# Optimization experiments

Hardware: AMD Instinct MI355X
Metric: run time of the kernel (lower is better)

Reference implementation:

```python
import jax, jax.numpy as jnp
import numpy as np

BN_EPS = 1e-5


def setup_inputs() -> dict:
    key = jax.random.key(0)
    k1, k2 = jax.random.split(key)
    B, IN, OUT = 16384, 2048, 2048
    x = jax.random.normal(k1, (B, IN), dtype=jnp.float32)
    weight = jax.random.normal(k2, (OUT, IN), dtype=jnp.float32) * 0.05
    gamma = jnp.ones((OUT,), dtype=jnp.float32)
    beta = jnp.zeros((OUT,), dtype=jnp.float32)
    return {"x": x, "weight": weight, "gamma": gamma, "beta": beta}


def reference(x, weight, gamma, beta):
    # Deterministic binarization: sign(w) in {-1, +1} (0 maps to +1)
    w_bin = jnp.where(weight >= 0, 1.0, -1.0).astype(weight.dtype)
    # Linear (no bias): y = x @ W_bin^T  -> [B, OUT]
    y = jnp.einsum("bi,oi->bo", x, w_bin)
    # BatchNorm1d, training mode: biased batch statistics over batch dim
    mean = jnp.mean(y, axis=0)
    var = jnp.mean(jnp.square(y - mean), axis=0)
    y = (y - mean) * (gamma * jax.lax.rsqrt(var + BN_EPS)) + beta
    # ReLU activation
    return jax.nn.relu(y)
```

## Files before the change

kernel.cpp:

```cpp
#include <hip/hip_runtime.h>
#include <stdint.h>

#define B_DIM   16384
#define IN_DIM  2048
#define OUT_DIM 2048
#define BN_EPS  1e-5f

typedef __bf16 bf16x8 __attribute__((ext_vector_type(8)));
typedef float  f32x4  __attribute__((ext_vector_type(4)));
typedef unsigned short u16x4 __attribute__((ext_vector_type(4)));
typedef unsigned short u16x8 __attribute__((ext_vector_type(8)));


__device__ __forceinline__ unsigned short f2bf_rne(float f) {
    unsigned u = __builtin_bit_cast(unsigned, f);
    return (unsigned short)((u + 0x7fffu + ((u >> 16) & 1u)) >> 16);
}
__device__ __forceinline__ float bf2f(unsigned short h) {
    unsigned u = ((unsigned)h) << 16;
    return __builtin_bit_cast(float, u);
}

__device__ __forceinline__ void gl_lds16(const __bf16* g, __bf16* l) {
    __builtin_amdgcn_global_load_lds(
        (const __attribute__((address_space(1))) unsigned int*)g,
        (__attribute__((address_space(3))) unsigned int*)l,
        16, 0, 0);
}

__global__ __launch_bounds__(256) void convert_x_kernel(
        const float4* __restrict__ x, u16x4* __restrict__ xb) {
    int id = blockIdx.x * 256 + threadIdx.x;
    float4 a = x[id];
    u16x4 o;
    o[0] = f2bf_rne(a.x); o[1] = f2bf_rne(a.y);
    o[2] = f2bf_rne(a.z); o[3] = f2bf_rne(a.w);
    xb[id] = o;
}

__global__ __launch_bounds__(256) void convert_w_kernel(
        const float4* __restrict__ w, u16x4* __restrict__ wb,
        float4* __restrict__ stats ) {
    int id = blockIdx.x * 256 + threadIdx.x;
    if (id < 1024) stats[id] = make_float4(0.f, 0.f, 0.f, 0.f);
    float4 a = w[id];
    u16x4 o;
    o[0] = (unsigned short)((a.x < 0.f) ? 0xBF80u : 0x3F80u);
    o[1] = (unsigned short)((a.y < 0.f) ? 0xBF80u : 0x3F80u);
    o[2] = (unsigned short)((a.z < 0.f) ? 0xBF80u : 0x3F80u);
    o[3] = (unsigned short)((a.w < 0.f) ? 0xBF80u : 0x3F80u);
    wb[id] = o;
}

template <bool BF16OUT>
__global__ __launch_bounds__(256, 2) void gemm_bn_kernel(
        const __bf16* __restrict__ A, const __bf16* __restrict__ Bw,
        unsigned short* __restrict__ Yb, float* __restrict__ Yf,
        float* __restrict__ colsum, float* __restrict__ colsumsq) {
    __shared__ __bf16 sA[128 * 32];
    __shared__ __bf16 sB[128 * 32];

    const int tid  = threadIdx.x;
    const int wave = tid >> 6;
    const int lane = tid & 63;
    const int wm = wave >> 1;
    const int wn = wave & 1;
    const int lr = lane & 15;
    const int lq = lane >> 4;

    const int b    = blockIdx.x;
    const int lb   = (b & 7) * 256 + (b >> 3);
    const int bm   = (lb >> 4) * 128;
    const int bn   = (lb & 15) * 128;

    const int srow = lane >> 2;
    const int scol = (lane & 3) * 8;
    const int chunk0 = wave * 2;
    const __bf16* ag0 = A  + (size_t)(bm + chunk0 * 16 + srow) * IN_DIM + scol;
    const __bf16* ag1 = ag0 + 16 * IN_DIM;
    const __bf16* bg0 = Bw + (size_t)(bn + chunk0 * 16 + srow) * IN_DIM + scol;
    const __bf16* bg1 = bg0 + 16 * IN_DIM;
    __bf16* la0 = sA + chunk0 * 512;
    __bf16* la1 = sA + (chunk0 + 1) * 512;
    __bf16* lb0 = sB + chunk0 * 512;
    __bf16* lb1 = sB + (chunk0 + 1) * 512;

    const int aoff = (wm * 64 + lr) * 32 + lq * 8;
    const int boff = (wn * 64 + lr) * 32 + lq * 8;

    f32x4 acc[4][4];
#pragma unroll
    for (int i = 0; i < 4; ++i)
#pragma unroll
        for (int j = 0; j < 4; ++j) {
            f32x4 z = {0.f, 0.f, 0.f, 0.f};
            acc[i][j] = z;
        }

    for (int k0 = 0; k0 < IN_DIM; k0 += 32) {
        __syncthreads();
        gl_lds16(ag0 + k0, la0);
        gl_lds16(ag1 + k0, la1);
        gl_lds16(bg0 + k0, lb0);
        gl_lds16(bg1 + k0, lb1);
        __syncthreads();

        bf16x8 av[4], bv[4];
#pragma unroll
        for (int i = 0; i < 4; ++i)
            av[i] = *(const bf16x8*)(sA + aoff + i * 512);
#pragma unroll
        for (int j = 0; j < 4; ++j)
            bv[j] = *(const bf16x8*)(sB + boff + j * 512);
#pragma unroll
        for (int i = 0; i < 4; ++i)
#pragma unroll
            for (int j = 0; j < 4; ++j)
                acc[i][j] = __builtin_amdgcn_mfma_f32_16x16x32_bf16(
                    av[i], bv[j], acc[i][j], 0, 0, 0);
    }

#pragma unroll
    for (int i = 0; i < 4; ++i) {
        int row0 = bm + wm * 64 + i * 16 + lq * 4;
#pragma unroll
        for (int r = 0; r < 4; ++r) {
            size_t base = (size_t)(row0 + r) * OUT_DIM + bn + wn * 64 + lr;
            if (BF16OUT) {
#pragma unroll
                for (int j = 0; j < 4; ++j)
                    Yb[base + j * 16] = f2bf_rne(acc[i][j][r]);
            } else {
#pragma unroll
                for (int j = 0; j < 4; ++j)
                    Yf[base + j * 16] = acc[i][j][r];
            }
        }
    }

#pragma unroll
    for (int j = 0; j < 4; ++j) {
        float s = 0.f, q = 0.f;
#pragma unroll
        for (int i = 0; i < 4; ++i)
#pragma unroll
            for (int r = 0; r < 4; ++r) {
                float v = acc[i][j][r];
                s += v;
                q += v * v;
            }
        s += __shfl_xor(s, 16); s += __shfl_xor(s, 32);
        q += __shfl_xor(q, 16); q += __shfl_xor(q, 32);
        if (lq == 0) {
            int col = bn + wn * 64 + j * 16 + lr;
            atomicAdd(&colsum[col], s);
            atomicAdd(&colsumsq[col], q);
        }
    }
}

__global__ __launch_bounds__(256) void finalize_kernel(
        const float* __restrict__ colsum, const float* __restrict__ colsumsq,
        const float* __restrict__ gamma, const float* __restrict__ beta,
        float* __restrict__ scale, float* __restrict__ bias) {
    int n = blockIdx.x * 256 + threadIdx.x;
    if (n < OUT_DIM) {
        const float inv = 1.f / (float)B_DIM;
        float mean = colsum[n] * inv;
        float var  = colsumsq[n] * inv - mean * mean;
        float sc   = gamma[n] * rsqrtf(var + BN_EPS);
        scale[n] = sc;
        bias[n]  = beta[n] - mean * sc;
    }
}

__global__ __launch_bounds__(256) void bn_relu_bf16_kernel(
        const u16x4* __restrict__ yb, float4* __restrict__ out,
        const float4* __restrict__ scale4, const float4* __restrict__ bias4) {
    int id = blockIdx.x * 256 + threadIdx.x;
    int c4 = id & (OUT_DIM / 4 - 1);
    u16x4 h = yb[id];
    float4 s = scale4[c4];
    float4 b = bias4[c4];
    float4 v;
    v.x = fmaxf(fmaf(bf2f(h[0]), s.x, b.x), 0.f);
    v.y = fmaxf(fmaf(bf2f(h[1]), s.y, b.y), 0.f);
    v.z = fmaxf(fmaf(bf2f(h[2]), s.z, b.z), 0.f);
    v.w = fmaxf(fmaf(bf2f(h[3]), s.w, b.w), 0.f);
    out[id] = v;
}

__global__ __launch_bounds__(256) void bn_relu_f32_kernel(
        float4* __restrict__ y, const float4* __restrict__ scale4,
        const float4* __restrict__ bias4) {
    int id = blockIdx.x * 256 + threadIdx.x;
    int c4 = id & (OUT_DIM / 4 - 1);
    float4 v = y[id];
    float4 s = scale4[c4];
    float4 b = bias4[c4];
    v.x = fmaxf(fmaf(v.x, s.x, b.x), 0.f);
    v.y = fmaxf(fmaf(v.y, s.y, b.y), 0.f);
    v.z = fmaxf(fmaf(v.z, s.z, b.z), 0.f);
    v.w = fmaxf(fmaf(v.w, s.w, b.w), 0.f);
    y[id] = v;
}

extern "C" void kernel_launch(void* const* d_in, const int* in_sizes, int n_in,
                              void* d_out, int out_size, void* d_ws, size_t ws_size,
                              hipStream_t stream) {
    const float* x     = (const float*)d_in[0];
    const float* w     = (const float*)d_in[1];
    const float* gamma = (const float*)d_in[2];
    const float* beta  = (const float*)d_in[3];
    float* out = (float*)d_out;

    char* ws = (char*)d_ws;
    const size_t XB_OFF = 0;
    const size_t WB_OFF = 67108864;
    const size_t YB_OFF = WB_OFF + 8388608;
    const size_t ST_OFF = YB_OFF + 67108864;
    const size_t NEED   = ST_OFF + 8192 * 4;

    __bf16* xb = (__bf16*)(ws + XB_OFF);
    __bf16* wb = (__bf16*)(ws + WB_OFF);
    unsigned short* yb = (unsigned short*)(ws + YB_OFF);
    bool use_bf16y = ws_size >= NEED;
    float* colsum = use_bf16y ? (float*)(ws + ST_OFF) : (float*)(ws + YB_OFF);
    float* colsumsq = colsum + 2048;
    float* scale    = colsum + 4096;
    float* bias     = colsum + 6144;

    convert_x_kernel<<<32768, 256, 0, stream>>>((const float4*)x, (u16x4*)xb);
    convert_w_kernel<<<4096, 256, 0, stream>>>((const float4*)w, (u16x4*)wb,
                                               (float4*)colsum);
    if (use_bf16y) {
        gemm_bn_kernel<true><<<2048, 256, 0, stream>>>(
            xb, wb, yb, out, colsum, colsumsq);
        finalize_kernel<<<8, 256, 0, stream>>>(colsum, colsumsq, gamma, beta,
                                               scale, bias);
        bn_relu_bf16_kernel<<<32768, 256, 0, stream>>>(
            (const u16x4*)yb, (float4*)out, (const float4*)scale,
            (const float4*)bias);
    } else {
        gemm_bn_kernel<false><<<2048, 256, 0, stream>>>(
            xb, wb, yb, out, colsum, colsumsq);
        finalize_kernel<<<8, 256, 0, stream>>>(colsum, colsumsq, gamma, beta,
                                               scale, bias);
        bn_relu_f32_kernel<<<32768, 256, 0, stream>>>(
            (float4*)out, (const float4*)scale, (const float4*)bias);
    }
}
```

Baseline: 406.9 us.

## Quantize activations to per-row int8 and use int8 MFMA for binary GEMM

Replaces the bf16 conversion of x with a per-row absmax int8 quantization kernel, and encodes the binarized weights as int8 ±1. The GEMM now uses the i32 16x16x64 int8 MFMA with a 64-wide K step, which halves the loop trip count and halves operand bytes. The row scale is applied in the epilogue before the bf16 store and the column statistics. The intent is to cut both matrix-core time and input conversion traffic. In exchange, activations are held at 8-bit precision, which adds quantization error to the outputs and the BN statistics, and the fp32 fallback path for small workspaces is removed.

```diff
diff --git a/kernel.cpp b/kernel.cpp
--- a/kernel.cpp
+++ b/kernel.cpp
@@ -6,10 +6,8 @@
 #define OUT_DIM 2048
 #define BN_EPS  1e-5f
 
-typedef __bf16 bf16x8 __attribute__((ext_vector_type(8)));
-typedef float  f32x4  __attribute__((ext_vector_type(4)));
+typedef int    i32x4 __attribute__((ext_vector_type(4)));
 typedef unsigned short u16x4 __attribute__((ext_vector_type(4)));
-typedef unsigned short u16x8 __attribute__((ext_vector_type(8)));
 
 
 __device__ __forceinline__ unsigned short f2bf_rne(float f) {
@@ -21,44 +19,65 @@
     return __builtin_bit_cast(float, u);
 }
 
-__device__ __forceinline__ void gl_lds16(const __bf16* g, __bf16* l) {
+__device__ __forceinline__ void gl_lds16(const void* g, void* l) {
     __builtin_amdgcn_global_load_lds(
         (const __attribute__((address_space(1))) unsigned int*)g,
         (__attribute__((address_space(3))) unsigned int*)l,
         16, 0, 0);
 }
 
-__global__ __launch_bounds__(256) void convert_x_kernel(
-        const float4* __restrict__ x, u16x4* __restrict__ xb) {
-    int id = blockIdx.x * 256 + threadIdx.x;
-    float4 a = x[id];
-    u16x4 o;
-    o[0] = f2bf_rne(a.x); o[1] = f2bf_rne(a.y);
-    o[2] = f2bf_rne(a.z); o[3] = f2bf_rne(a.w);
-    xb[id] = o;
+__device__ __forceinline__ int pack4(float a, float b, float c, float d, float inv) {
+    int q0 = (int)rintf(a * inv) & 255;
+    int q1 = (int)rintf(b * inv) & 255;
+    int q2 = (int)rintf(c * inv) & 255;
+    int q3 = (int)rintf(d * inv) & 255;
+    return q0 | (q1 << 8) | (q2 << 16) | (q3 << 24);
+}
+
+__global__ __launch_bounds__(256) void quantize_x_kernel(
+        const float4* __restrict__ x4, int* __restrict__ xq,
+        float* __restrict__ scales) {
+    __shared__ float wmax[4];
+    const int row = blockIdx.x;
+    const int t = threadIdx.x;
+    const float4* xr = x4 + (size_t)row * 512;
+    float4 a = xr[t];
+    float4 b = xr[t + 256];
+    float m = fmaxf(fmaxf(fabsf(a.x), fabsf(a.y)), fmaxf(fabsf(a.z), fabsf(a.w)));
+    m = fmaxf(m, fmaxf(fmaxf(fabsf(b.x), fabsf(b.y)), fmaxf(fabsf(b.z), fabsf(b.w))));
+#pragma unroll
+    for (int off = 32; off >= 1; off >>= 1) m = fmaxf(m, __shfl_xor(m, off));
+    if ((t & 63) == 0) wmax[t >> 6] = m;
+    __syncthreads();
+    m = fmaxf(fmaxf(wmax[0], wmax[1]), fmaxf(wmax[2], wmax[3]));
+    m = fmaxf(m, 1e-20f);
+    const float inv = 127.0f / m;
+    if (t == 0) scales[row] = m * (1.0f / 127.0f);
+    int* xo = xq + (size_t)row * 512;
+    xo[t]       = pack4(a.x, a.y, a.z, a.w, inv);
+    xo[t + 256] = pack4(b.x, b.y, b.z, b.w, inv);
 }
 
 __global__ __launch_bounds__(256) void convert_w_kernel(
-        const float4* __restrict__ w, u16x4* __restrict__ wb,
+        const float4* __restrict__ w, int* __restrict__ wq,
         float4* __restrict__ stats ) {
     int id = blockIdx.x * 256 + threadIdx.x;
     if (id < 1024) stats[id] = make_float4(0.f, 0.f, 0.f, 0.f);
     float4 a = w[id];
-    u16x4 o;
-    o[0] = (unsigned short)((a.x < 0.f) ? 0xBF80u : 0x3F80u);
-    o[1] = (unsigned short)((a.y < 0.f) ? 0xBF80u : 0x3F80u);
-    o[2] = (unsigned short)((a.z < 0.f) ? 0xBF80u : 0x3F80u);
-    o[3] = (unsigned short)((a.w < 0.f) ? 0xBF80u : 0x3F80u);
-    wb[id] = o;
-}
-
-template <bool BF16OUT>
+    int b0 = (a.x < 0.f) ? 0xFF : 0x01;
+    int b1 = (a.y < 0.f) ? 0xFF : 0x01;
+    int b2 = (a.z < 0.f) ? 0xFF : 0x01;
+    int b3 = (a.w < 0.f) ? 0xFF : 0x01;
+    wq[id] = b0 | (b1 << 8) | (b2 << 16) | (b3 << 24);
+}
+
 __global__ __launch_bounds__(256, 2) void gemm_bn_kernel(
-        const __bf16* __restrict__ A, const __bf16* __restrict__ Bw,
-        unsigned short* __restrict__ Yb, float* __restrict__ Yf,
+        const char* __restrict__ A, const char* __restrict__ Bw,
+        const float* __restrict__ scales,
+        unsigned short* __restrict__ Yb,
         float* __restrict__ colsum, float* __restrict__ colsumsq) {
-    __shared__ __bf16 sA[128 * 32];
-    __shared__ __bf16 sB[128 * 32];
+    __shared__ char sA[128 * 64];
+    __shared__ char sB[128 * 64];
 
     const int tid  = threadIdx.x;
     const int wave = tid >> 6;
@@ -68,36 +87,36 @@
     const int lr = lane & 15;
     const int lq = lane >> 4;
 
-    const int b    = blockIdx.x;
-    const int lb   = (b & 7) * 256 + (b >> 3);
-    const int bm   = (lb >> 4) * 128;
-    const int bn   = (lb & 15) * 128;
+    const int b  = blockIdx.x;
+    const int lb = (b & 7) * 256 + (b >> 3);
+    const int bm = (lb >> 4) * 128;
+    const int bn = (lb & 15) * 128;
 
     const int srow = lane >> 2;
-    const int scol = (lane & 3) * 8;
+    const int scol = (lane & 3) * 16;
     const int chunk0 = wave * 2;
-    const __bf16* ag0 = A  + (size_t)(bm + chunk0 * 16 + srow) * IN_DIM + scol;
-    const __bf16* ag1 = ag0 + 16 * IN_DIM;
-    const __bf16* bg0 = Bw + (size_t)(bn + chunk0 * 16 + srow) * IN_DIM + scol;
-    const __bf16* bg1 = bg0 + 16 * IN_DIM;
-    __bf16* la0 = sA + chunk0 * 512;
-    __bf16* la1 = sA + (chunk0 + 1) * 512;
-    __bf16* lb0 = sB + chunk0 * 512;
-    __bf16* lb1 = sB + (chunk0 + 1) * 512;
-
-    const int aoff = (wm * 64 + lr) * 32 + lq * 8;
-    const int boff = (wn * 64 + lr) * 32 + lq * 8;
-
-    f32x4 acc[4][4];
+    const char* ag0 = A  + (size_t)(bm + chunk0 * 16 + srow) * IN_DIM + scol;
+    const char* ag1 = ag0 + 16 * IN_DIM;
+    const char* bg0 = Bw + (size_t)(bn + chunk0 * 16 + srow) * IN_DIM + scol;
+    const char* bg1 = bg0 + 16 * IN_DIM;
+    char* la0 = sA + chunk0 * 1024;
+    char* la1 = sA + (chunk0 + 1) * 1024;
+    char* lb0 = sB + chunk0 * 1024;
+    char* lb1 = sB + (chunk0 + 1) * 1024;
+
+    const int aoff = (wm * 64 + lr) * 64 + lq * 16;
+    const int boff = (wn * 64 + lr) * 64 + lq * 16;
+
+    i32x4 acc[4][4];
 #pragma unroll
     for (int i = 0; i < 4; ++i)
 #pragma unroll
         for (int j = 0; j < 4; ++j) {
-            f32x4 z = {0.f, 0.f, 0.f, 0.f};
+            i32x4 z = {0, 0, 0, 0};
             acc[i][j] = z;
         }
 
-    for (int k0 = 0; k0 < IN_DIM; k0 += 32) {
+    for (int k0 = 0; k0 < IN_DIM; k0 += 64) {
         __syncthreads();
         gl_lds16(ag0 + k0, la0);
         gl_lds16(ag1 + k0, la1);
@@ -105,50 +124,47 @@
         gl_lds16(bg1 + k0, lb1);
         __syncthreads();
 
-        bf16x8 av[4], bv[4];
+        i32x4 av[4], bv[4];
 #pragma unroll
         for (int i = 0; i < 4; ++i)
-            av[i] = *(const bf16x8*)(sA + aoff + i * 512);
+            av[i] = *(const i32x4*)(sA + aoff + i * 1024);
 #pragma unroll
         for (int j = 0; j < 4; ++j)
-            bv[j] = *(const bf16x8*)(sB + boff + j * 512);
+            bv[j] = *(const i32x4*)(sB + boff + j * 1024);
 #pragma unroll
         for (int i = 0; i < 4; ++i)
 #pragma unroll
             for (int j = 0; j < 4; ++j)
-                acc[i][j] = __builtin_amdgcn_mfma_f32_16x16x32_bf16(
+                acc[i][j] = __builtin_amdgcn_mfma_i32_16x16x64_i8(
                     av[i], bv[j], acc[i][j], 0, 0, 0);
     }
 
+    float colS[4], colQ[4];
+#pragma unroll
+    for (int j = 0; j < 4; ++j) { colS[j] = 0.f; colQ[j] = 0.f; }
+
 #pragma unroll
     for (int i = 0; i < 4; ++i) {
-        int row0 = bm + wm * 64 + i * 16 + lq * 4;
+        const int row0 = bm + wm * 64 + i * 16 + lq * 4;
+        float sc[4];
+#pragma unroll
+        for (int r = 0; r < 4; ++r) sc[r] = scales[row0 + r];
 #pragma unroll
         for (int r = 0; r < 4; ++r) {
             size_t base = (size_t)(row0 + r) * OUT_DIM + bn + wn * 64 + lr;
-            if (BF16OUT) {
-#pragma unroll
-                for (int j = 0; j < 4; ++j)
-                    Yb[base + j * 16] = f2bf_rne(acc[i][j][r]);
-            } else {
-#pragma unroll
-                for (int j = 0; j < 4; ++j)
-                    Yf[base + j * 16] = acc[i][j][r];
+#pragma unroll
+            for (int j = 0; j < 4; ++j) {
+                float v = (float)acc[i][j][r] * sc[r];
+                Yb[base + j * 16] = f2bf_rne(v);
+                colS[j] += v;
+                colQ[j] += v * v;
             }
         }
     }
 
 #pragma unroll
     for (int j = 0; j < 4; ++j) {
-        float s = 0.f, q = 0.f;
-#pragma unroll
-        for (int i = 0; i < 4; ++i)
-#pragma unroll
-            for (int r = 0; r < 4; ++r) {
-                float v = acc[i][j][r];
-                s += v;
-                q += v * v;
-            }
+        float s = colS[j], q = colQ[j];
         s += __shfl_xor(s, 16); s += __shfl_xor(s, 32);
         q += __shfl_xor(q, 16); q += __shfl_xor(q, 32);
         if (lq == 0) {
@@ -190,21 +206,6 @@
     out[id] = v;
 }
 
-__global__ __launch_bounds__(256) void bn_relu_f32_kernel(
-        float4* __restrict__ y, const float4* __restrict__ scale4,
-        const float4* __restrict__ bias4) {
-    int id = blockIdx.x * 256 + threadIdx.x;
-    int c4 = id & (OUT_DIM / 4 - 1);
-    float4 v = y[id];
-    float4 s = scale4[c4];
-    float4 b = bias4[c4];
-    v.x = fmaxf(fmaf(v.x, s.x, b.x), 0.f);
-    v.y = fmaxf(fmaf(v.y, s.y, b.y), 0.f);
-    v.z = fmaxf(fmaf(v.z, s.z, b.z), 0.f);
-    v.w = fmaxf(fmaf(v.w, s.w, b.w), 0.f);
-    y[id] = v;
-}
-
 extern "C" void kernel_launch(void* const* d_in, const int* in_sizes, int n_in,
                               void* d_out, int out_size, void* d_ws, size_t ws_size,
                               hipStream_t stream) {
@@ -215,38 +216,30 @@
     float* out = (float*)d_out;
 
     char* ws = (char*)d_ws;
-    const size_t XB_OFF = 0;
-    const size_t WB_OFF = 67108864;
-    const size_t YB_OFF = WB_OFF + 8388608;
-    const size_t ST_OFF = YB_OFF + 67108864;
-    const size_t NEED   = ST_OFF + 8192 * 4;
-
-    __bf16* xb = (__bf16*)(ws + XB_OFF);
-    __bf16* wb = (__bf16*)(ws + WB_OFF);
+    const size_t XQ_OFF = 0;
+    const size_t WQ_OFF = XQ_OFF + (size_t)B_DIM * IN_DIM;
+    const size_t YB_OFF = WQ_OFF + (size_t)OUT_DIM * IN_DIM;
+    const size_t ST_OFF = YB_OFF + (size_t)B_DIM * OUT_DIM * 2;
+    const size_t SC_OFF = ST_OFF + 8192 * 4;
+
+    char* xq = ws + XQ_OFF;
+    char* wq = ws + WQ_OFF;
     unsigned short* yb = (unsigned short*)(ws + YB_OFF);
-    bool use_bf16y = ws_size >= NEED;
-    float* colsum = use_bf16y ? (float*)(ws + ST_OFF) : (float*)(ws + YB_OFF);
+    float* colsum   = (float*)(ws + ST_OFF);
     float* colsumsq = colsum + 2048;
     float* scale    = colsum + 4096;
     float* bias     = colsum + 6144;
-
-    convert_x_kernel<<<32768, 256, 0, stream>>>((const float4*)x, (u16x4*)xb);
-    convert_w_kernel<<<4096, 256, 0, stream>>>((const float4*)w, (u16x4*)wb,
-                                               (float4*)colsum);
-    if (use_bf16y) {
-        gemm_bn_kernel<true><<<2048, 256, 0, stream>>>(
-            xb, wb, yb, out, colsum, colsumsq);
-        finalize_kernel<<<8, 256, 0, stream>>>(colsum, colsumsq, gamma, beta,
-                                               scale, bias);
-        bn_relu_bf16_kernel<<<32768, 256, 0, stream>>>(
-            (const u16x4*)yb, (float4*)out, (const float4*)scale,
-            (const float4*)bias);
-    } else {
-        gemm_bn_kernel<false><<<2048, 256, 0, stream>>>(
-            xb, wb, yb, out, colsum, colsumsq);
-        finalize_kernel<<<8, 256, 0, stream>>>(colsum, colsumsq, gamma, beta,
-                                               scale, bias);
-        bn_relu_f32_kernel<<<32768, 256, 0, stream>>>(
-            (float4*)out, (const float4*)scale, (const float4*)bias);
-    }
-}
+    float* scales   = (float*)(ws + SC_OFF);
+
+    quantize_x_kernel<<<B_DIM, 256, 0, stream>>>(
+        (const float4*)x, (int*)xq, scales);
+    convert_w_kernel<<<4096, 256, 0, stream>>>(
+        (const float4*)w, (int*)wq, (float4*)colsum);
+    gemm_bn_kernel<<<2048, 256, 0, stream>>>(
+        xq, wq, scales, yb, colsum, colsumsq);
+    finalize_kernel<<<8, 256, 0, stream>>>(
+        colsum, colsumsq, gamma, beta, scale, bias);
+    bn_relu_bf16_kernel<<<32768, 256, 0, stream>>>(
+        (const u16x4*)yb, (float4*)out, (const float4*)scale,
+        (const float4*)bias);
+}
```

After: 342.6 us. -15.8%, faster.
